# Kernel optimization log

Measured on AMD Instinct MI355X. Metric: run time of the kernel, lower is better.

## Reference

```python
import jax, jax.numpy as jnp
import numpy as np

T, B, IN, H, OUT = 345, 128, 13, 128, 9

# snnTorch ATan surrogate spike: forward = heaviside(x), backward = 1/(1+(pi*x)^2) (alpha=2)
@jax.custom_vjp
def spike_fn(x):
    return (x > 0).astype(x.dtype)

def _spike_fwd(x):
    return spike_fn(x), x

def _spike_bwd(x, g):
    return (g / (1.0 + (jnp.pi * x) ** 2),)

spike_fn.defvjp(_spike_fwd, _spike_bwd)


def setup_inputs() -> dict:
    key = jax.random.key(0)
    ks = jax.random.split(key, 5)
    x = jax.random.normal(ks[0], (B, IN, T), dtype=jnp.float32)
    # PyTorch Linear init: U(-1/sqrt(fan_in), 1/sqrt(fan_in))
    lim1 = 1.0 / np.sqrt(IN)
    lim2 = 1.0 / np.sqrt(H)
    W1 = jax.random.uniform(ks[1], (H, IN), minval=-lim1, maxval=lim1, dtype=jnp.float32)
    b1 = jax.random.uniform(ks[2], (H,), minval=-lim1, maxval=lim1, dtype=jnp.float32)
    W2 = jax.random.uniform(ks[3], (OUT, H), minval=-lim2, maxval=lim2, dtype=jnp.float32)
    b2 = jax.random.uniform(ks[4], (OUT,), minval=-lim2, maxval=lim2, dtype=jnp.float32)
    beta1 = jnp.float32(0.9)
    thr1 = jnp.float32(1.0)
    beta2 = jnp.float32(0.9)
    thr2 = jnp.float32(1.0)
    return {"x": x, "W1": W1, "b1": b1, "W2": W2, "b2": b2,
            "beta1": beta1, "thr1": thr1, "beta2": beta2, "thr2": thr2}


def reference(x, W1, b1, W2, b2, beta1, thr1, beta2, thr2):
    # Precompute fc1 for all steps: (T, B, H)
    cur1_all = jnp.einsum('bct,hc->tbh', x, W1) + b1
    bt1 = jnp.clip(beta1, 0.0, 1.0)
    bt2 = jnp.clip(beta2, 0.0, 1.0)

    def step(carry, cur1):
        mem1, mem2 = carry
        mem1 = bt1 * mem1 + cur1                 # leaky integrate
        spk1 = spike_fn(mem1 - thr1)             # fire
        mem1 = mem1 - spk1 * thr1                # subtract reset
        cur2 = spk1 @ W2.T + b2                  # (B, OUT)
        mem2 = bt2 * mem2 + cur2
        spk2 = spike_fn(mem2 - thr2)
        mem2 = mem2 - spk2 * thr2
        return (mem1, mem2), (spk2, mem2)

    init = (jnp.zeros((B, H), x.dtype), jnp.zeros((B, OUT), x.dtype))
    _, (spk_rec, mem_rec) = jax.lax.scan(step, init, cur1_all)
    return spk_rec, mem_rec  # each (T, B, OUT)
```

## Files before the change

### kernel.cpp

```cpp
#include <hip/hip_runtime.h>

#define T_STEPS 345
#define B_SZ    128
#define IN_SZ   13
#define H_SZ    128
#define OUT_SZ  9
#define XPITCH  16
#define TPAD    384
#define NBO     (B_SZ * OUT_SZ)
#define MASK_BYTES (B_SZ * T_STEPS * 2 * 8)

__global__ __launch_bounds__(128, 1)
void k1_spikes(const float* __restrict__ x, const float* __restrict__ W1,
               const float* __restrict__ b1, const float* __restrict__ beta1p,
               const float* __restrict__ thr1p,
               unsigned long long* __restrict__ masks)
{
    const int b   = blockIdx.x;
    const int tid = threadIdx.x;

    __shared__ float xst[(T_STEPS + 3) * XPITCH];

    const float* xb = x + (size_t)b * (IN_SZ * T_STEPS);
    for (int i = tid; i < IN_SZ * T_STEPS; i += 128) {
        const int c = i / T_STEPS;
        const int t = i - c * T_STEPS;
        xst[t * XPITCH + c] = xb[i];
    }

    const float bt1 = fminf(fmaxf(beta1p[0], 0.0f), 1.0f);
    const float th1 = thr1p[0];

    float w1r[IN_SZ];
#pragma unroll
    for (int c = 0; c < IN_SZ; ++c) w1r[c] = W1[tid * IN_SZ + c];
    const float b1r = b1[tid];

    float mem1 = 0.0f;
    unsigned long long* mp = masks + (size_t)b * (T_STEPS * 2) + (tid >> 6);
    const bool store_lane = (tid & 63) == 0;

    __syncthreads();

    const float4* xq = (const float4*)xst;
    float4 a0 = xq[0], a1 = xq[1], a2 = xq[2]; float a3 = xst[12];
    float4 c0 = xq[4], c1 = xq[5], c2 = xq[6]; float c3 = xst[XPITCH + 12];

    int t = 0;
    for (; t < T_STEPS - 1; t += 2) {
        const float xa[IN_SZ] = { a0.x,a0.y,a0.z,a0.w, a1.x,a1.y,a1.z,a1.w,
                                  a2.x,a2.y,a2.z,a2.w, a3 };
        const float xc[IN_SZ] = { c0.x,c0.y,c0.z,c0.w, c1.x,c1.y,c1.z,c1.w,
                                  c2.x,c2.y,c2.z,c2.w, c3 };
        a0 = xq[(t+2)*4+0]; a1 = xq[(t+2)*4+1]; a2 = xq[(t+2)*4+2]; a3 = xst[(t+2)*XPITCH+12];
        c0 = xq[(t+3)*4+0]; c1 = xq[(t+3)*4+1]; c2 = xq[(t+3)*4+2]; c3 = xst[(t+3)*XPITCH+12];

        float cura = b1r, curb = b1r;
#pragma unroll
        for (int c = 0; c < IN_SZ; ++c) {
            cura = fmaf(xa[c], w1r[c], cura);
            curb = fmaf(xc[c], w1r[c], curb);
        }

        mem1 = fmaf(bt1, mem1, cura);
        const bool pa = mem1 > th1;
        const unsigned long long ma = __ballot(pa);
        mem1 = fmaf(pa ? -1.0f : 0.0f, th1, mem1);
        if (store_lane) mp[0] = ma;

        mem1 = fmaf(bt1, mem1, curb);
        const bool pb = mem1 > th1;
        const unsigned long long mb = __ballot(pb);
        mem1 = fmaf(pb ? -1.0f : 0.0f, th1, mem1);
        if (store_lane) mp[2] = mb;

        mp += 4;
    }
    {
        const float xa[IN_SZ] = { a0.x,a0.y,a0.z,a0.w, a1.x,a1.y,a1.z,a1.w,
                                  a2.x,a2.y,a2.z,a2.w, a3 };
        float cura = b1r;
#pragma unroll
        for (int c = 0; c < IN_SZ; ++c) cura = fmaf(xa[c], w1r[c], cura);
        mem1 = fmaf(bt1, mem1, cura);
        const bool pa = mem1 > th1;
        const unsigned long long ma = __ballot(pa);
        if (store_lane) mp[0] = ma;
    }
}

__global__ __launch_bounds__(256, 1)
void k2_gemm(const unsigned long long* __restrict__ masks,
             const float* __restrict__ W2, const float* __restrict__ b2,
             float* __restrict__ cur2)
{
    const int gw   = blockIdx.x * 4 + (threadIdx.x >> 6);
    const int lane = threadIdx.x & 63;
    const int bo   = gw / 6;
    const int w    = gw - bo * 6;
    const int b    = bo / 9;
    const int o    = bo - b * 9;
    const int t    = w * 64 + lane;
    const int tc   = (t < T_STEPS) ? t : (T_STEPS - 1);

    const uint4 mm = *(const uint4*)((const char*)masks +
                                     ((size_t)b * T_STEPS + tc) * 16);

    const float* __restrict__ w2row = W2 + o * H_SZ;
    float acc = 0.0f;
#pragma unroll
    for (int h = 0; h < 32; ++h)
        acc = fmaf((float)((mm.x >> h) & 1u), w2row[h], acc);
#pragma unroll
    for (int h = 0; h < 32; ++h)
        acc = fmaf((float)((mm.y >> h) & 1u), w2row[32 + h], acc);
#pragma unroll
    for (int h = 0; h < 32; ++h)
        acc = fmaf((float)((mm.z >> h) & 1u), w2row[64 + h], acc);
#pragma unroll
    for (int h = 0; h < 32; ++h)
        acc = fmaf((float)((mm.w >> h) & 1u), w2row[96 + h], acc);

    cur2[(size_t)bo * TPAD + t] = acc + b2[o];
}

__global__ __launch_bounds__(64, 1)
void k3_scan2(const float* __restrict__ cur2, const float* __restrict__ beta2p,
              const float* __restrict__ thr2p, float* __restrict__ out)
{
    const int lid = blockIdx.x * 64 + threadIdx.x;
    const float bt2 = fminf(fmaxf(beta2p[0], 0.0f), 1.0f);
    const float th2 = thr2p[0];

    const float4* __restrict__ src = (const float4*)(cur2 + (size_t)lid * TPAD);
    float* __restrict__ out_spk = out + lid;
    float* __restrict__ out_mem = out + (size_t)T_STEPS * NBO + lid;

    float mem2 = 0.0f;

    float4 f0 = src[0], f1 = src[1], f2 = src[2], f3 = src[3];

    for (int g = 0; g < 88; g += 4) {
        const float4 u0 = f0, u1 = f1, u2 = f2, u3 = f3;
        f0 = src[g + 4]; f1 = src[g + 5]; f2 = src[g + 6]; f3 = src[g + 7];

        const float4 us[4] = { u0, u1, u2, u3 };
#pragma unroll
        for (int j = 0; j < 4; ++j) {
            const float vv[4] = { us[j].x, us[j].y, us[j].z, us[j].w };
#pragma unroll
            for (int k = 0; k < 4; ++k) {
                const int tt = (g + j) * 4 + k;
                mem2 = fmaf(bt2, mem2, vv[k]);
                const float s2 = (mem2 > th2) ? 1.0f : 0.0f;
                mem2 = fmaf(-s2, th2, mem2);
                if (tt < T_STEPS) {
                    out_spk[(size_t)tt * NBO] = s2;
                    out_mem[(size_t)tt * NBO] = mem2;
                }
            }
        }
    }
}

extern "C" void kernel_launch(void* const* d_in, const int* in_sizes, int n_in,
                              void* d_out, int out_size, void* d_ws, size_t ws_size,
                              hipStream_t stream) {
    const float* x     = (const float*)d_in[0];
    const float* W1    = (const float*)d_in[1];
    const float* b1    = (const float*)d_in[2];
    const float* W2    = (const float*)d_in[3];
    const float* b2    = (const float*)d_in[4];
    const float* beta1 = (const float*)d_in[5];
    const float* thr1  = (const float*)d_in[6];
    const float* beta2 = (const float*)d_in[7];
    const float* thr2  = (const float*)d_in[8];
    float* out = (float*)d_out;

    char* ws = (char*)d_ws;
    unsigned long long* masks = (unsigned long long*)ws;
    float* cur2 = (float*)(ws + MASK_BYTES);

    k1_spikes<<<dim3(B_SZ), dim3(128), 0, stream>>>(x, W1, b1, beta1, thr1, masks);
    k2_gemm  <<<dim3(1728), dim3(256), 0, stream>>>(masks, W2, b2, cur2);
    k3_scan2 <<<dim3(NBO / 64), dim3(64), 0, stream>>>(cur2, beta2, thr2, out);
}
```

Before: 124.7 us.

## Transpose cur2 to time-major and chunk-prefetch the second-layer scan

The intermediate cur2 buffer changes from per-(batch,output) rows to a time-major layout, so lanes in the scan kernel read consecutive addresses at each step. The scan kernel now loads 16-step chunks into registers with double buffering and batches the spike and membrane stores per chunk. The aim is to replace the scan's strided per-thread float4 loads with coalesced loads and to hide load latency in the serial recurrence. In exchange, the GEMM kernel's cur2 writes become strided across lanes.

```diff
diff --git a/kernel.cpp b/kernel.cpp
--- a/kernel.cpp
+++ b/kernel.cpp
@@ -8,6 +8,7 @@
 #define XPITCH  16
 #define TPAD    384
 #define NBO     (B_SZ * OUT_SZ)
+#define NCHUNK  22
 #define MASK_BYTES (B_SZ * T_STEPS * 2 * 8)
 
 __global__ __launch_bounds__(128, 1)
@@ -121,7 +122,7 @@
     for (int h = 0; h < 32; ++h)
         acc = fmaf((float)((mm.w >> h) & 1u), w2row[96 + h], acc);
 
-    cur2[(size_t)bo * TPAD + t] = acc + b2[o];
+    cur2[(size_t)t * NBO + bo] = acc + b2[o];
 }
 
 __global__ __launch_bounds__(64, 1)
@@ -132,32 +133,63 @@
     const float bt2 = fminf(fmaxf(beta2p[0], 0.0f), 1.0f);
     const float th2 = thr2p[0];
 
-    const float4* __restrict__ src = (const float4*)(cur2 + (size_t)lid * TPAD);
+    const float* __restrict__ src = cur2 + lid;
     float* __restrict__ out_spk = out + lid;
     float* __restrict__ out_mem = out + (size_t)T_STEPS * NBO + lid;
 
     float mem2 = 0.0f;
 
-    float4 f0 = src[0], f1 = src[1], f2 = src[2], f3 = src[3];
-
-    for (int g = 0; g < 88; g += 4) {
-        const float4 u0 = f0, u1 = f1, u2 = f2, u3 = f3;
-        f0 = src[g + 4]; f1 = src[g + 5]; f2 = src[g + 6]; f3 = src[g + 7];
-
-        const float4 us[4] = { u0, u1, u2, u3 };
-#pragma unroll
-        for (int j = 0; j < 4; ++j) {
-            const float vv[4] = { us[j].x, us[j].y, us[j].z, us[j].w };
-#pragma unroll
-            for (int k = 0; k < 4; ++k) {
-                const int tt = (g + j) * 4 + k;
-                mem2 = fmaf(bt2, mem2, vv[k]);
-                const float s2 = (mem2 > th2) ? 1.0f : 0.0f;
-                mem2 = fmaf(-s2, th2, mem2);
-                if (tt < T_STEPS) {
-                    out_spk[(size_t)tt * NBO] = s2;
-                    out_mem[(size_t)tt * NBO] = mem2;
-                }
+    float A[16], Bb[16];
+#pragma unroll
+    for (int j = 0; j < 16; ++j) A[j]  = src[(size_t)j * NBO];
+#pragma unroll
+    for (int j = 0; j < 16; ++j) Bb[j] = src[(size_t)(16 + j) * NBO];
+
+    float sE[16], mE[16], sO[16], mO[16];
+
+    for (int c = 0; c < NCHUNK; c += 2) {
+#pragma unroll
+        for (int j = 0; j < 16; ++j) {
+            mem2 = fmaf(bt2, mem2, A[j]);
+            const float sp = (mem2 > th2) ? 1.0f : 0.0f;
+            mem2 = fmaf(-sp, th2, mem2);
+            sE[j] = sp; mE[j] = mem2;
+        }
+        const int cn = (c + 2 < NCHUNK) ? (c + 2) : c;
+#pragma unroll
+        for (int j = 0; j < 16; ++j) A[j] = src[(size_t)(cn * 16 + j) * NBO];
+        {
+            const size_t base = (size_t)c * 16 * NBO;
+#pragma unroll
+            for (int j = 0; j < 16; ++j) {
+                out_spk[base + (size_t)j * NBO] = sE[j];
+                out_mem[base + (size_t)j * NBO] = mE[j];
+            }
+        }
+
+#pragma unroll
+        for (int j = 0; j < 16; ++j) {
+            mem2 = fmaf(bt2, mem2, Bb[j]);
+            const float sp = (mem2 > th2) ? 1.0f : 0.0f;
+            mem2 = fmaf(-sp, th2, mem2);
+            sO[j] = sp; mO[j] = mem2;
+        }
+        const int cn2 = (c + 3 < NCHUNK) ? (c + 3) : c;
+#pragma unroll
+        for (int j = 0; j < 16; ++j) Bb[j] = src[(size_t)(cn2 * 16 + j) * NBO];
+        if (c + 1 < NCHUNK - 1) {
+            const size_t base = (size_t)(c + 1) * 16 * NBO;
+#pragma unroll
+            for (int j = 0; j < 16; ++j) {
+                out_spk[base + (size_t)j * NBO] = sO[j];
+                out_mem[base + (size_t)j * NBO] = mO[j];
+            }
+        } else {
+            const size_t base = (size_t)(c + 1) * 16 * NBO;
+#pragma unroll
+            for (int j = 0; j < 9; ++j) {
+                out_spk[base + (size_t)j * NBO] = sO[j];
+                out_mem[base + (size_t)j * NBO] = mO[j];
             }
         }
     }
```

After: 128.6 us. 1.03x slower.
